# Kernel tuning notes

Hardware: AMD Instinct MI355X
Metric: run time of the kernel (lower is better)

Reference implementation:

```python
import jax, jax.numpy as jnp
import numpy as np

B, S, D, H = 2, 2048, 1024, 16

def setup_inputs() -> dict:
    key = jax.random.key(0)
    ks = jax.random.split(key, 5)
    s = 0.02
    return {
        "x": jax.random.normal(ks[0], (B, S, D), dtype=jnp.float32),
        "Wq": jax.random.normal(ks[1], (D, D), dtype=jnp.float32) * s,
        "bq": jnp.zeros((D,), dtype=jnp.float32),
        "Wk": jax.random.normal(ks[2], (D, D), dtype=jnp.float32) * s,
        "bk": jnp.zeros((D,), dtype=jnp.float32),
        "Wv": jax.random.normal(ks[3], (D, D), dtype=jnp.float32) * s,
        "bv": jnp.zeros((D,), dtype=jnp.float32),
        "Wp": jax.random.normal(ks[4], (D, D), dtype=jnp.float32) * s,
        "bp": jnp.zeros((D,), dtype=jnp.float32),
    }

def reference(x, Wq, bq, Wk, bk, Wv, bv, Wp, bp):
    b, s, d = x.shape
    hd = d // H
    # QKV projections, split into heads: [b, H, s, hd]
    q = (x @ Wq.T + bq).reshape(b, s, H, hd).transpose(0, 2, 1, 3)
    k = (x @ Wk.T + bk).reshape(b, s, H, hd).transpose(0, 2, 1, 3)
    v = (x @ Wv.T + bv).reshape(b, s, H, hd).transpose(0, 2, 1, 3)
    # NOTE: original scales by 1/sqrt(embedding_size), not head_dim
    att = jnp.einsum("bhqd,bhkd->bhqk", q, k) / jnp.sqrt(jnp.float32(d))
    causal = jnp.tril(jnp.ones((s, s), dtype=bool))
    att = jnp.where(causal[None, None], att, -jnp.inf)
    att = jax.nn.softmax(att, axis=-1)
    y = jnp.einsum("bhqk,bhkd->bhqd", att, v)
    y = y.transpose(0, 2, 1, 3).reshape(b, s, d)
    return y @ Wp.T + bp
```

## Files before the change

kernel.cpp:

```cpp
#include <hip/hip_runtime.h>
#include <hip/hip_bf16.h>

#define B_  2
#define S_  2048
#define D_  1024
#define H_  16
#define HD_ 64

typedef float  f32x4 __attribute__((ext_vector_type(4)));
typedef __bf16 bf16x8 __attribute__((ext_vector_type(8)));

__device__ __forceinline__ unsigned short f2bf(float f) {
    __bf16 h = (__bf16)f;
    return __builtin_bit_cast(unsigned short, h);
}
__device__ __forceinline__ float bf2f(unsigned short u) {
    return (float)__builtin_bit_cast(__bf16, u);
}

__device__ __forceinline__ void gload_lds16(const unsigned short* g, unsigned short* l) {
    __builtin_amdgcn_global_load_lds(
        (const __attribute__((address_space(1))) unsigned int*)g,
        (__attribute__((address_space(3))) unsigned int*)l, 16, 0, 0);
}

__global__ __launch_bounds__(256) void cvt5(
    const float* __restrict__ x,  const float* __restrict__ wq,
    const float* __restrict__ wk, const float* __restrict__ wv,
    const float* __restrict__ wp, const float* __restrict__ bq,
    const float* __restrict__ bk, const float* __restrict__ bv,
    unsigned short* __restrict__ xb, unsigned short* __restrict__ wqkv,
    unsigned short* __restrict__ wpb, float* __restrict__ bcat)
{
    const int bid = blockIdx.x;
    if (bid >= 8192) {
        const float* s = (bid == 8192) ? bq : (bid == 8193) ? bk : bv;
        const int i = threadIdx.x * 4;
        *reinterpret_cast<float4*>(bcat + (bid - 8192) * 1024 + i) =
            *reinterpret_cast<const float4*>(s + i);
        return;
    }
    const float* src; unsigned short* dst; int off;
    if (bid < 4096)      { src = x;  dst = xb;              off = bid * 1024; }
    else if (bid < 5120) { src = wq; dst = wqkv;            off = (bid - 4096) * 1024; }
    else if (bid < 6144) { src = wk; dst = wqkv + (1<<20);  off = (bid - 5120) * 1024; }
    else if (bid < 7168) { src = wv; dst = wqkv + (2<<20);  off = (bid - 6144) * 1024; }
    else                 { src = wp; dst = wpb;             off = (bid - 7168) * 1024; }
    const int i = off + threadIdx.x * 4;
    float4 v = *reinterpret_cast<const float4*>(src + i);
    ushort4 o;
    o.x = f2bf(v.x); o.y = f2bf(v.y); o.z = f2bf(v.z); o.w = f2bf(v.w);
    *reinterpret_cast<ushort4*>(dst + i) = o;
}

__global__ __launch_bounds__(256, 3) void gemm128_qkv(
    const unsigned short* __restrict__ A,
    const unsigned short* __restrict__ Bm,
    const float* __restrict__ bias,
    void* __restrict__ C0, void* __restrict__ C1, void* __restrict__ C2,
    int M, int N, int K)
{
    __shared__ unsigned short As[128 * 64];
    __shared__ unsigned short Bs[128 * 64];
    const int tid  = threadIdx.x;
    const int lane = tid & 63;
    const int w    = tid >> 6;
    const int wm   = w >> 1, wn = w & 1;
    const int m0   = blockIdx.x << 7, n0 = blockIdx.y << 7;
    const int l15  = lane & 15, l4 = lane >> 4;
    const int r8   = lane >> 3;
    const int c8   = (lane & 7) << 3;

    f32x4 acc[4][4] = {};

    for (int k0 = 0; k0 < K; k0 += 64) {
        if (k0) __syncthreads();
        #pragma unroll
        for (int i = 0; i < 4; ++i) {
            const int row = i * 32 + w * 8;
            gload_lds16(A  + (size_t)(m0 + row + r8) * K + k0 + c8, As + row * 64);
            gload_lds16(Bm + (size_t)(n0 + row + r8) * K + k0 + c8, Bs + row * 64);
        }
        __syncthreads();
        #pragma unroll
        for (int kk = 0; kk < 2; ++kk) {
            bf16x8 af[4], bf[4];
            #pragma unroll
            for (int mi = 0; mi < 4; ++mi)
                af[mi] = *reinterpret_cast<const bf16x8*>(&As[(wm * 64 + mi * 16 + l15) * 64 + kk * 32 + l4 * 8]);
            #pragma unroll
            for (int ni = 0; ni < 4; ++ni)
                bf[ni] = *reinterpret_cast<const bf16x8*>(&Bs[(wn * 64 + ni * 16 + l15) * 64 + kk * 32 + l4 * 8]);
            #pragma unroll
            for (int mi = 0; mi < 4; ++mi)
                #pragma unroll
                for (int ni = 0; ni < 4; ++ni)
                    acc[mi][ni] = __builtin_amdgcn_mfma_f32_16x16x32_bf16(af[mi], bf[ni], acc[mi][ni], 0, 0, 0);
        }
    }

    const int region = n0 >> 10;
    #pragma unroll
    for (int mi = 0; mi < 4; ++mi) {
        #pragma unroll
        for (int ni = 0; ni < 4; ++ni) {
            const int colg = n0 + wn * 64 + ni * 16 + l15;
            const float bv = bias[colg];
            const int rowb = m0 + wm * 64 + mi * 16 + l4 * 4;
            const int cl = colg & 1023;
            if (region < 2) {
                unsigned short* C = (unsigned short*)(region ? C1 : C0);
                #pragma unroll
                for (int j = 0; j < 4; ++j)
                    C[(size_t)(rowb + j) * 1024 + cl] = f2bf(acc[mi][ni][j] + bv);
            } else {
                ushort4 pk;
                pk.x = f2bf(acc[mi][ni][0] + bv);
                pk.y = f2bf(acc[mi][ni][1] + bv);
                pk.z = f2bf(acc[mi][ni][2] + bv);
                pk.w = f2bf(acc[mi][ni][3] + bv);
                const int bb = rowb >> 11, s = rowb & (S_ - 1);
                unsigned short* vt = (unsigned short*)C2 +
                    ((size_t)(bb * H_ + (cl >> 6)) * HD_ + (cl & 63)) * S_ + s;
                *reinterpret_cast<ushort4*>(vt) = pk;
            }
        }
    }
}

__global__ __launch_bounds__(256, 2) void gemm64_proj(
    const unsigned short* __restrict__ A,
    const unsigned short* __restrict__ Bm,
    const float* __restrict__ bias,
    float* __restrict__ C,
    int M, int N, int K)
{
    __shared__ unsigned short As[64 * 64];
    __shared__ unsigned short Bs[128 * 64];
    const int tid  = threadIdx.x;
    const int lane = tid & 63;
    const int w    = tid >> 6;
    const int m0   = blockIdx.x << 6, n0 = blockIdx.y << 7;
    const int l15  = lane & 15, l4 = lane >> 4;
    const int r8   = lane >> 3;
    const int c8   = (lane & 7) << 3;

    f32x4 acc[4][2] = {};

    for (int k0 = 0; k0 < K; k0 += 64) {
        if (k0) __syncthreads();
        #pragma unroll
        for (int i = 0; i < 6; ++i) {
            const int c = w * 6 + i;
            if (c < 8)
                gload_lds16(A  + (size_t)(m0 + c * 8 + r8) * K + k0 + c8, As + c * 512);
            else
                gload_lds16(Bm + (size_t)(n0 + (c - 8) * 8 + r8) * K + k0 + c8, Bs + (c - 8) * 512);
        }
        __syncthreads();
        #pragma unroll
        for (int kk = 0; kk < 2; ++kk) {
            bf16x8 af[4], bf[2];
            #pragma unroll
            for (int mi = 0; mi < 4; ++mi)
                af[mi] = *reinterpret_cast<const bf16x8*>(&As[(mi * 16 + l15) * 64 + kk * 32 + l4 * 8]);
            #pragma unroll
            for (int ni = 0; ni < 2; ++ni)
                bf[ni] = *reinterpret_cast<const bf16x8*>(&Bs[(w * 32 + ni * 16 + l15) * 64 + kk * 32 + l4 * 8]);
            #pragma unroll
            for (int mi = 0; mi < 4; ++mi)
                #pragma unroll
                for (int ni = 0; ni < 2; ++ni)
                    acc[mi][ni] = __builtin_amdgcn_mfma_f32_16x16x32_bf16(af[mi], bf[ni], acc[mi][ni], 0, 0, 0);
        }
    }

    #pragma unroll
    for (int mi = 0; mi < 4; ++mi) {
        #pragma unroll
        for (int ni = 0; ni < 2; ++ni) {
            const int colg = n0 + w * 32 + ni * 16 + l15;
            const float bv = bias[colg];
            const int rowb = m0 + mi * 16 + l4 * 4;
            #pragma unroll
            for (int j = 0; j < 4; ++j)
                C[(size_t)(rowb + j) * N + colg] = acc[mi][ni][j] + bv;
        }
    }
}

#define SC_ 0.04508422f
__global__ __launch_bounds__(64, 2) void attn8(
    const unsigned short* __restrict__ qb,
    const unsigned short* __restrict__ kb,
    const unsigned short* __restrict__ vt,
    unsigned short* __restrict__ opart,
    float* __restrict__ lpart)
{
    __shared__ unsigned short Plds[32][88];

    const int lane = threadIdx.x;
    const int l15  = lane & 15, l4 = lane >> 4;

    const int bid  = blockIdx.x;
    const int xcd  = bid & 7;
    const int idx  = bid >> 3;
    const int hb   = xcd * 4 + (idx >> 7);
    const int rem  = idx & 127;
    const int sp   = rem >> 6;
    const int j    = rem & 63;
    const int j32  = j & 31;
    const int qi   = ((j >> 5) & 1) ? j32 : 63 - j32;
    const int h    = hb & 15, b = hb >> 4;

    const int q0w  = qi * 32;
    const size_t baseTok = (size_t)b * S_;
    const unsigned short* kgh = kb + baseTok * D_ + h * HD_;
    const unsigned short* vth = vt + (size_t)(b * H_ + h) * HD_ * S_;

    const int nkv  = (q0w + 95) >> 6;
    const int half = (nkv + 1) >> 1;
    const int t0   = sp ? half : 0;
    const int t1   = sp ? nkv  : half;

    bf16x8 qf[2][2];
    #pragma unroll
    for (int m = 0; m < 2; ++m)
        #pragma unroll
        for (int kh = 0; kh < 2; ++kh)
            qf[m][kh] = *reinterpret_cast<const bf16x8*>(
                qb + (baseTok + q0w + m * 16 + l15) * D_ + h * HD_ + kh * 32 + l4 * 8);

    f32x4 o_acc[2][4] = {};
    float l_part[2][4] = {};

    if (t0 < t1) {
        bf16x8 kf[4][2];
        #pragma unroll
        for (int kvb = 0; kvb < 4; ++kvb)
            #pragma unroll
            for (int kh = 0; kh < 2; ++kh)
                kf[kvb][kh] = *reinterpret_cast<const bf16x8*>(
                    kgh + (size_t)(t0 * 64 + kvb * 16 + l15) * D_ + kh * 32 + l4 * 8);

        for (int t = t0; t < t1; ++t) {
            const int kv0 = t << 6;
            const bool last = (t == nkv - 1);

            f32x4 s0[4] = {}, s1[4] = {};
            __builtin_amdgcn_s_setprio(1);
            #pragma unroll
            for (int kvb = 0; kvb < 4; ++kvb)
                #pragma unroll
                for (int kh = 0; kh < 2; ++kh)
                    s0[kvb] = __builtin_amdgcn_mfma_f32_16x16x32_bf16(
                        qf[0][kh], kf[kvb][kh], s0[kvb], 0, 0, 0);
            #pragma unroll
            for (int kvb = 0; kvb < 4; ++kvb)
                #pragma unroll
                for (int kh = 0; kh < 2; ++kh)
                    s1[kvb] = __builtin_amdgcn_mfma_f32_16x16x32_bf16(
                        qf[1][kh], kf[kvb][kh], s1[kvb], 0, 0, 0);
            __builtin_amdgcn_s_setprio(0);

            if (t + 1 < t1) {
                #pragma unroll
                for (int kvb = 0; kvb < 4; ++kvb)
                    #pragma unroll
                    for (int kh = 0; kh < 2; ++kh)
                        kf[kvb][kh] = *reinterpret_cast<const bf16x8*>(
                            kgh + (size_t)(kv0 + 64 + kvb * 16 + l15) * D_ + kh * 32 + l4 * 8);
            }

            bf16x8 vf0[4];
            #pragma unroll
            for (int nb = 0; nb < 4; ++nb)
                vf0[nb] = *reinterpret_cast<const bf16x8*>(
                    vth + (size_t)(nb * 16 + l15) * S_ + kv0 + l4 * 8);

            const int r = l4 * 4;
            if (!last) {
                #pragma unroll
                for (int jj = 0; jj < 4; ++jj) {
                    float p0 = exp2f(s0[0][jj] * SC_), p1 = exp2f(s0[1][jj] * SC_);
                    float p2 = exp2f(s0[2][jj] * SC_), p3 = exp2f(s0[3][jj] * SC_);
                    l_part[0][jj] += (p0 + p1) + (p2 + p3);
                    Plds[r + jj][l15]      = f2bf(p0);
                    Plds[r + jj][16 + l15] = f2bf(p1);
                    Plds[r + jj][32 + l15] = f2bf(p2);
                    Plds[r + jj][48 + l15] = f2bf(p3);
                }
                #pragma unroll
                for (int jj = 0; jj < 4; ++jj) {
                    float p0 = exp2f(s1[0][jj] * SC_), p1 = exp2f(s1[1][jj] * SC_);
                    float p2 = exp2f(s1[2][jj] * SC_), p3 = exp2f(s1[3][jj] * SC_);
                    l_part[1][jj] += (p0 + p1) + (p2 + p3);
                    Plds[16 + r + jj][l15]      = f2bf(p0);
                    Plds[16 + r + jj][16 + l15] = f2bf(p1);
                    Plds[16 + r + jj][32 + l15] = f2bf(p2);
                    Plds[16 + r + jj][48 + l15] = f2bf(p3);
                }
            } else {
                #pragma unroll
                for (int jj = 0; jj < 4; ++jj) {
                    const int rowg = q0w + r + jj;
                    float p[4];
                    #pragma unroll
                    for (int kvb = 0; kvb < 4; ++kvb) {
                        const bool ok = (kv0 + kvb * 16 + l15 <= rowg);
                        p[kvb] = ok ? exp2f(s0[kvb][jj] * SC_) : 0.f;
                        Plds[r + jj][kvb * 16 + l15] = f2bf(p[kvb]);
                    }
                    l_part[0][jj] += (p[0] + p[1]) + (p[2] + p[3]);
                }
                #pragma unroll
                for (int jj = 0; jj < 4; ++jj) {
                    const int rowg = q0w + 16 + r + jj;
                    float p[4];
                    #pragma unroll
                    for (int kvb = 0; kvb < 4; ++kvb) {
                        const bool ok = (kv0 + kvb * 16 + l15 <= rowg);
                        p[kvb] = ok ? exp2f(s1[kvb][jj] * SC_) : 0.f;
                        Plds[16 + r + jj][kvb * 16 + l15] = f2bf(p[kvb]);
                    }
                    l_part[1][jj] += (p[0] + p[1]) + (p[2] + p[3]);
                }
            }

            bf16x8 vf1[4];
            #pragma unroll
            for (int nb = 0; nb < 4; ++nb)
                vf1[nb] = *reinterpret_cast<const bf16x8*>(
                    vth + (size_t)(nb * 16 + l15) * S_ + kv0 + 32 + l4 * 8);

            {
                bf16x8 pf0 = *reinterpret_cast<const bf16x8*>(&Plds[l15][l4 * 8]);
                bf16x8 pf1 = *reinterpret_cast<const bf16x8*>(&Plds[16 + l15][l4 * 8]);
                __builtin_amdgcn_s_setprio(1);
                #pragma unroll
                for (int nb = 0; nb < 4; ++nb) {
                    o_acc[0][nb] = __builtin_amdgcn_mfma_f32_16x16x32_bf16(pf0, vf0[nb], o_acc[0][nb], 0, 0, 0);
                    o_acc[1][nb] = __builtin_amdgcn_mfma_f32_16x16x32_bf16(pf1, vf0[nb], o_acc[1][nb], 0, 0, 0);
                }
                __builtin_amdgcn_s_setprio(0);
            }
            {
                bf16x8 pf0 = *reinterpret_cast<const bf16x8*>(&Plds[l15][32 + l4 * 8]);
                bf16x8 pf1 = *reinterpret_cast<const bf16x8*>(&Plds[16 + l15][32 + l4 * 8]);
                __builtin_amdgcn_s_setprio(1);
                #pragma unroll
                for (int nb = 0; nb < 4; ++nb) {
                    o_acc[0][nb] = __builtin_amdgcn_mfma_f32_16x16x32_bf16(pf0, vf1[nb], o_acc[0][nb], 0, 0, 0);
                    o_acc[1][nb] = __builtin_amdgcn_mfma_f32_16x16x32_bf16(pf1, vf1[nb], o_acc[1][nb], 0, 0, 0);
                }
                __builtin_amdgcn_s_setprio(0);
            }
        }
    }

    const int slot = (hb * 64 + qi) * 2 + sp;
    float l[8];
    #pragma unroll
    for (int m = 0; m < 2; ++m)
        #pragma unroll
        for (int jj = 0; jj < 4; ++jj)
            l[m * 4 + jj] = l_part[m][jj];
    #pragma unroll
    for (int st = 1; st <= 8; st <<= 1) {
        float tv[8];
        #pragma unroll
        for (int i = 0; i < 8; ++i) tv[i] = __shfl_xor(l[i], st);
        #pragma unroll
        for (int i = 0; i < 8; ++i) l[i] += tv[i];
    }
    if (l15 == 0) {
        float* lp = lpart + slot * 32;
        #pragma unroll
        for (int m = 0; m < 2; ++m)
            #pragma unroll
            for (int jj = 0; jj < 4; ++jj)
                lp[m * 16 + l4 * 4 + jj] = l[m * 4 + jj];
    }
    unsigned short* op = opart + (size_t)slot * 2048;
    #pragma unroll
    for (int m = 0; m < 2; ++m)
        #pragma unroll
        for (int nb = 0; nb < 4; ++nb)
            #pragma unroll
            for (int jj = 0; jj < 4; ++jj)
                op[(m * 16 + l4 * 4 + jj) * 64 + nb * 16 + l15] = f2bf(o_acc[m][nb][jj]);
}

__global__ __launch_bounds__(64) void attn_combine(
    const unsigned short* __restrict__ opart,
    const float* __restrict__ lpart,
    unsigned short* __restrict__ yb)
{
    const int g   = blockIdx.x;
    const int hb  = g >> 6, qi = g & 63;
    const int b   = hb >> 4, h = hb & 15;
    const int lane = threadIdx.x;
    const unsigned short* op0 = opart + (size_t)(g * 2) * 2048;
    const unsigned short* op1 = op0 + 2048;
    const float* lp0 = lpart + g * 2 * 32;
    const float* lp1 = lp0 + 32;
    #pragma unroll 4
    for (int row = 0; row < 32; ++row) {
        const float o = bf2f(op0[row * 64 + lane]) + bf2f(op1[row * 64 + lane]);
        const float l = lp0[row] + lp1[row];
        yb[((size_t)(b * S_ + qi * 32 + row)) * D_ + h * HD_ + lane] = f2bf(o / l);
    }
}

extern "C" void kernel_launch(void* const* d_in, const int* in_sizes, int n_in,
                              void* d_out, int out_size, void* d_ws, size_t ws_size,
                              hipStream_t stream)
{
    const float* x  = (const float*)d_in[0];
    const float* Wq = (const float*)d_in[1];
    const float* bq = (const float*)d_in[2];
    const float* Wk = (const float*)d_in[3];
    const float* bk = (const float*)d_in[4];
    const float* Wv = (const float*)d_in[5];
    const float* bv = (const float*)d_in[6];
    const float* Wp = (const float*)d_in[7];
    const float* bp = (const float*)d_in[8];

    char* ws = (char*)d_ws;
    const size_t MB = 1024 * 1024;
    unsigned short* xb    = (unsigned short*)(ws);
    unsigned short* wqkvb = (unsigned short*)(ws + 8 * MB);
    unsigned short* opart = (unsigned short*)(ws);
    unsigned short* qbuf  = (unsigned short*)(ws + 16 * MB);
    unsigned short* kbuf  = (unsigned short*)(ws + 24 * MB);
    unsigned short* vtbf  = (unsigned short*)(ws + 32 * MB);
    unsigned short* ybuf  = (unsigned short*)(ws + 40 * MB);
    unsigned short* wpb   = (unsigned short*)(ws + 48 * MB);
    float*          bcat  = (float*)(ws + 50 * MB);
    float*          lpart = (float*)(ws + 50 * MB + 65536);

    const int M = B_ * S_;

    cvt5<<<8195, 256, 0, stream>>>(x, Wq, Wk, Wv, Wp, bq, bk, bv, xb, wqkvb, wpb, bcat);

    gemm128_qkv<<<dim3(M / 128, 3072 / 128, 1), 256, 0, stream>>>(
        xb, wqkvb, bcat, qbuf, kbuf, vtbf, M, 3072, D_);

    attn8<<<4096, 64, 0, stream>>>(qbuf, kbuf, vtbf, opart, lpart);
    attn_combine<<<2048, 64, 0, stream>>>(opart, lpart, ybuf);

    gemm64_proj<<<dim3(M / 64, D_ / 128, 1), 256, 0, stream>>>(
        ybuf, wpb, bp, (float*)d_out, M, D_, D_);
}
```

Baseline: 235.4 us.

## Balance causal attention work with variable KV splits per query tile

Replaces the fixed two-way KV split per query tile with a variable split: short tiles run unsplit, medium tiles split in two and long tiles in three. Blocks are ordered heaviest-first within each head group. The change also drops the empty split blocks and evens out per-block work to reduce tail imbalance. The combine kernel now sums a variable number of partials, and the V loads for both halves are hoisted together, which raises register pressure.

Result: slower. 252.7 us (+7.3%).

```diff
diff --git a/kernel.cpp b/kernel.cpp
--- a/kernel.cpp
+++ b/kernel.cpp
@@ -190,7 +190,7 @@
 }
 
 #define SC_ 0.04508422f
-__global__ __launch_bounds__(64, 2) void attn8(
+__global__ __launch_bounds__(64, 2) void attn9(
     const unsigned short* __restrict__ qb,
     const unsigned short* __restrict__ kb,
     const unsigned short* __restrict__ vt,
@@ -205,24 +205,25 @@
     const int bid  = blockIdx.x;
     const int xcd  = bid & 7;
     const int idx  = bid >> 3;
-    const int hb   = xcd * 4 + (idx >> 7);
-    const int rem  = idx & 127;
-    const int sp   = rem >> 6;
-    const int j    = rem & 63;
-    const int j32  = j & 31;
-    const int qi   = ((j >> 5) & 1) ? j32 : 63 - j32;
-    const int h    = hb & 15, b = hb >> 4;
+    const int hb   = xcd * 4 + idx / 126;
+    const int srr  = idx % 126;
+    const int slot = 125 - srr;
+    int qi, part, ns;
+    if (slot < 22)      { qi = slot; part = 0; ns = 1; }
+    else if (slot < 66) { const int u = slot - 22; qi = 22 + (u >> 1); part = u & 1; ns = 2; }
+    else                { const int u = slot - 66; const int q3 = u / 3; qi = 44 + q3; part = u - q3 * 3; ns = 3; }
+    const int h = hb & 15, b = hb >> 4;
 
     const int q0w  = qi * 32;
+    const int nkv  = (qi >> 1) + 1;
+    const int len  = nkv / ns, rem = nkv % ns;
+    const int t0   = part * len + (part < rem ? part : rem);
+    const int t1   = t0 + len + (part < rem ? 1 : 0);
+
     const size_t baseTok = (size_t)b * S_;
     const unsigned short* kgh = kb + baseTok * D_ + h * HD_;
     const unsigned short* vth = vt + (size_t)(b * H_ + h) * HD_ * S_;
 
-    const int nkv  = (q0w + 95) >> 6;
-    const int half = (nkv + 1) >> 1;
-    const int t0   = sp ? half : 0;
-    const int t1   = sp ? nkv  : half;
-
     bf16x8 qf[2][2];
     #pragma unroll
     for (int m = 0; m < 2; ++m)
@@ -234,131 +235,127 @@
     f32x4 o_acc[2][4] = {};
     float l_part[2][4] = {};
 
-    if (t0 < t1) {
-        bf16x8 kf[4][2];
+    bf16x8 kf[4][2];
+    #pragma unroll
+    for (int kvb = 0; kvb < 4; ++kvb)
+        #pragma unroll
+        for (int kh = 0; kh < 2; ++kh)
+            kf[kvb][kh] = *reinterpret_cast<const bf16x8*>(
+                kgh + (size_t)(t0 * 64 + kvb * 16 + l15) * D_ + kh * 32 + l4 * 8);
+
+    for (int t = t0; t < t1; ++t) {
+        const int kv0 = t << 6;
+        const bool last = (t == nkv - 1);
+
+        f32x4 s0[4] = {}, s1[4] = {};
+        __builtin_amdgcn_s_setprio(1);
         #pragma unroll
         for (int kvb = 0; kvb < 4; ++kvb)
             #pragma unroll
             for (int kh = 0; kh < 2; ++kh)
-                kf[kvb][kh] = *reinterpret_cast<const bf16x8*>(
-                    kgh + (size_t)(t0 * 64 + kvb * 16 + l15) * D_ + kh * 32 + l4 * 8);
-
-        for (int t = t0; t < t1; ++t) {
-            const int kv0 = t << 6;
-            const bool last = (t == nkv - 1);
-
-            f32x4 s0[4] = {}, s1[4] = {};
+                s0[kvb] = __builtin_amdgcn_mfma_f32_16x16x32_bf16(
+                    qf[0][kh], kf[kvb][kh], s0[kvb], 0, 0, 0);
+        #pragma unroll
+        for (int kvb = 0; kvb < 4; ++kvb)
+            #pragma unroll
+            for (int kh = 0; kh < 2; ++kh)
+                s1[kvb] = __builtin_amdgcn_mfma_f32_16x16x32_bf16(
+                    qf[1][kh], kf[kvb][kh], s1[kvb], 0, 0, 0);
+        __builtin_amdgcn_s_setprio(0);
+
+        if (t + 1 < t1) {
+            #pragma unroll
+            for (int kvb = 0; kvb < 4; ++kvb)
+                #pragma unroll
+                for (int kh = 0; kh < 2; ++kh)
+                    kf[kvb][kh] = *reinterpret_cast<const bf16x8*>(
+                        kgh + (size_t)(kv0 + 64 + kvb * 16 + l15) * D_ + kh * 32 + l4 * 8);
+        }
+
+        bf16x8 vf0[4], vf1[4];
+        #pragma unroll
+        for (int nb = 0; nb < 4; ++nb)
+            vf0[nb] = *reinterpret_cast<const bf16x8*>(
+                vth + (size_t)(nb * 16 + l15) * S_ + kv0 + l4 * 8);
+        #pragma unroll
+        for (int nb = 0; nb < 4; ++nb)
+            vf1[nb] = *reinterpret_cast<const bf16x8*>(
+                vth + (size_t)(nb * 16 + l15) * S_ + kv0 + 32 + l4 * 8);
+
+        const int r = l4 * 4;
+        if (!last) {
+            #pragma unroll
+            for (int jj = 0; jj < 4; ++jj) {
+                float p0 = exp2f(s0[0][jj] * SC_), p1 = exp2f(s0[1][jj] * SC_);
+                float p2 = exp2f(s0[2][jj] * SC_), p3 = exp2f(s0[3][jj] * SC_);
+                l_part[0][jj] += (p0 + p1) + (p2 + p3);
+                Plds[r + jj][l15]      = f2bf(p0);
+                Plds[r + jj][16 + l15] = f2bf(p1);
+                Plds[r + jj][32 + l15] = f2bf(p2);
+                Plds[r + jj][48 + l15] = f2bf(p3);
+            }
+            #pragma unroll
+            for (int jj = 0; jj < 4; ++jj) {
+                float p0 = exp2f(s1[0][jj] * SC_), p1 = exp2f(s1[1][jj] * SC_);
+                float p2 = exp2f(s1[2][jj] * SC_), p3 = exp2f(s1[3][jj] * SC_);
+                l_part[1][jj] += (p0 + p1) + (p2 + p3);
+                Plds[16 + r + jj][l15]      = f2bf(p0);
+                Plds[16 + r + jj][16 + l15] = f2bf(p1);
+                Plds[16 + r + jj][32 + l15] = f2bf(p2);
+                Plds[16 + r + jj][48 + l15] = f2bf(p3);
+            }
+        } else {
+            #pragma unroll
+            for (int jj = 0; jj < 4; ++jj) {
+                const int rowg = q0w + r + jj;
+                float p[4];
+                #pragma unroll
+                for (int kvb = 0; kvb < 4; ++kvb) {
+                    const bool ok = (kv0 + kvb * 16 + l15 <= rowg);
+                    p[kvb] = ok ? exp2f(s0[kvb][jj] * SC_) : 0.f;
+                    Plds[r + jj][kvb * 16 + l15] = f2bf(p[kvb]);
+                }
+                l_part[0][jj] += (p[0] + p[1]) + (p[2] + p[3]);
+            }
+            #pragma unroll
+            for (int jj = 0; jj < 4; ++jj) {
+                const int rowg = q0w + 16 + r + jj;
+                float p[4];
+                #pragma unroll
+                for (int kvb = 0; kvb < 4; ++kvb) {
+                    const bool ok = (kv0 + kvb * 16 + l15 <= rowg);
+                    p[kvb] = ok ? exp2f(s1[kvb][jj] * SC_) : 0.f;
+                    Plds[16 + r + jj][kvb * 16 + l15] = f2bf(p[kvb]);
+                }
+                l_part[1][jj] += (p[0] + p[1]) + (p[2] + p[3]);
+            }
+        }
+
+        {
+            bf16x8 pf0 = *reinterpret_cast<const bf16x8*>(&Plds[l15][l4 * 8]);
+            bf16x8 pf1 = *reinterpret_cast<const bf16x8*>(&Plds[16 + l15][l4 * 8]);
             __builtin_amdgcn_s_setprio(1);
             #pragma unroll
-            for (int kvb = 0; kvb < 4; ++kvb)
-                #pragma unroll
-                for (int kh = 0; kh < 2; ++kh)
-                    s0[kvb] = __builtin_amdgcn_mfma_f32_16x16x32_bf16(
-                        qf[0][kh], kf[kvb][kh], s0[kvb], 0, 0, 0);
-            #pragma unroll
-            for (int kvb = 0; kvb < 4; ++kvb)
-                #pragma unroll
-                for (int kh = 0; kh < 2; ++kh)
-                    s1[kvb] = __builtin_amdgcn_mfma_f32_16x16x32_bf16(
-                        qf[1][kh], kf[kvb][kh], s1[kvb], 0, 0, 0);
+            for (int nb = 0; nb < 4; ++nb) {
+                o_acc[0][nb] = __builtin_amdgcn_mfma_f32_16x16x32_bf16(pf0, vf0[nb], o_acc[0][nb], 0, 0, 0);
+                o_acc[1][nb] = __builtin_amdgcn_mfma_f32_16x16x32_bf16(pf1, vf0[nb], o_acc[1][nb], 0, 0, 0);
+            }
             __builtin_amdgcn_s_setprio(0);
-
-            if (t + 1 < t1) {
-                #pragma unroll
-                for (int kvb = 0; kvb < 4; ++kvb)
-                    #pragma unroll
-                    for (int kh = 0; kh < 2; ++kh)
-                        kf[kvb][kh] = *reinterpret_cast<const bf16x8*>(
-                            kgh + (size_t)(kv0 + 64 + kvb * 16 + l15) * D_ + kh * 32 + l4 * 8);
-            }
-
-            bf16x8 vf0[4];
-            #pragma unroll
-            for (int nb = 0; nb < 4; ++nb)
-                vf0[nb] = *reinterpret_cast<const bf16x8*>(
-                    vth + (size_t)(nb * 16 + l15) * S_ + kv0 + l4 * 8);
-
-            const int r = l4 * 4;
-            if (!last) {
-                #pragma unroll
-                for (int jj = 0; jj < 4; ++jj) {
-                    float p0 = exp2f(s0[0][jj] * SC_), p1 = exp2f(s0[1][jj] * SC_);
-                    float p2 = exp2f(s0[2][jj] * SC_), p3 = exp2f(s0[3][jj] * SC_);
-                    l_part[0][jj] += (p0 + p1) + (p2 + p3);
-                    Plds[r + jj][l15]      = f2bf(p0);
-                    Plds[r + jj][16 + l15] = f2bf(p1);
-                    Plds[r + jj][32 + l15] = f2bf(p2);
-                    Plds[r + jj][48 + l15] = f2bf(p3);
-                }
-                #pragma unroll
-                for (int jj = 0; jj < 4; ++jj) {
-                    float p0 = exp2f(s1[0][jj] * SC_), p1 = exp2f(s1[1][jj] * SC_);
-                    float p2 = exp2f(s1[2][jj] * SC_), p3 = exp2f(s1[3][jj] * SC_);
-                    l_part[1][jj] += (p0 + p1) + (p2 + p3);
-                    Plds[16 + r + jj][l15]      = f2bf(p0);
-                    Plds[16 + r + jj][16 + l15] = f2bf(p1);
-                    Plds[16 + r + jj][32 + l15] = f2bf(p2);
-                    Plds[16 + r + jj][48 + l15] = f2bf(p3);
-                }
-            } else {
-                #pragma unroll
-                for (int jj = 0; jj < 4; ++jj) {
-                    const int rowg = q0w + r + jj;
-                    float p[4];
-                    #pragma unroll
-                    for (int kvb = 0; kvb < 4; ++kvb) {
-                        const bool ok = (kv0 + kvb * 16 + l15 <= rowg);
-                        p[kvb] = ok ? exp2f(s0[kvb][jj] * SC_) : 0.f;
-                        Plds[r + jj][kvb * 16 + l15] = f2bf(p[kvb]);
-                    }
-                    l_part[0][jj] += (p[0] + p[1]) + (p[2] + p[3]);
-                }
-                #pragma unroll
-                for (int jj = 0; jj < 4; ++jj) {
-                    const int rowg = q0w + 16 + r + jj;
-                    float p[4];
-                    #pragma unroll
-                    for (int kvb = 0; kvb < 4; ++kvb) {
-                        const bool ok = (kv0 + kvb * 16 + l15 <= rowg);
-                        p[kvb] = ok ? exp2f(s1[kvb][jj] * SC_) : 0.f;
-                        Plds[16 + r + jj][kvb * 16 + l15] = f2bf(p[kvb]);
-                    }
-                    l_part[1][jj] += (p[0] + p[1]) + (p[2] + p[3]);
-                }
-            }
-
-            bf16x8 vf1[4];
-            #pragma unroll
-            for (int nb = 0; nb < 4; ++nb)
-                vf1[nb] = *reinterpret_cast<const bf16x8*>(
-                    vth + (size_t)(nb * 16 + l15) * S_ + kv0 + 32 + l4 * 8);
-
-            {
-                bf16x8 pf0 = *reinterpret_cast<const bf16x8*>(&Plds[l15][l4 * 8]);
-                bf16x8 pf1 = *reinterpret_cast<const bf16x8*>(&Plds[16 + l15][l4 * 8]);
-                __builtin_amdgcn_s_setprio(1);
-                #pragma unroll
-                for (int nb = 0; nb < 4; ++nb) {
-                    o_acc[0][nb] = __builtin_amdgcn_mfma_f32_16x16x32_bf16(pf0, vf0[nb], o_acc[0][nb], 0, 0, 0);
-                    o_acc[1][nb] = __builtin_amdgcn_mfma_f32_16x16x32_bf16(pf1, vf0[nb], o_acc[1][nb], 0, 0, 0);
-                }
-                __builtin_amdgcn_s_setprio(0);
-            }
-            {
-                bf16x8 pf0 = *reinterpret_cast<const bf16x8*>(&Plds[l15][32 + l4 * 8]);
-                bf16x8 pf1 = *reinterpret_cast<const bf16x8*>(&Plds[16 + l15][32 + l4 * 8]);
-                __builtin_amdgcn_s_setprio(1);
-                #pragma unroll
-                for (int nb = 0; nb < 4; ++nb) {
-                    o_acc[0][nb] = __builtin_amdgcn_mfma_f32_16x16x32_bf16(pf0, vf1[nb], o_acc[0][nb], 0, 0, 0);
-                    o_acc[1][nb] = __builtin_amdgcn_mfma_f32_16x16x32_bf16(pf1, vf1[nb], o_acc[1][nb], 0, 0, 0);
-                }
-                __builtin_amdgcn_s_setprio(0);
-            }
-        }
-    }
-
-    const int slot = (hb * 64 + qi) * 2 + sp;
+        }
+        {
+            bf16x8 pf0 = *reinterpret_cast<const bf16x8*>(&Plds[l15][32 + l4 * 8]);
+            bf16x8 pf1 = *reinterpret_cast<const bf16x8*>(&Plds[16 + l15][32 + l4 * 8]);
+            __builtin_amdgcn_s_setprio(1);
+            #pragma unroll
+            for (int nb = 0; nb < 4; ++nb) {
+                o_acc[0][nb] = __builtin_amdgcn_mfma_f32_16x16x32_bf16(pf0, vf1[nb], o_acc[0][nb], 0, 0, 0);
+                o_acc[1][nb] = __builtin_amdgcn_mfma_f32_16x16x32_bf16(pf1, vf1[nb], o_acc[1][nb], 0, 0, 0);
+            }
+            __builtin_amdgcn_s_setprio(0);
+        }
+    }
+
+    const int gslot = hb * 126 + slot;
     float l[8];
     #pragma unroll
     for (int m = 0; m < 2; ++m)
@@ -374,14 +371,14 @@
         for (int i = 0; i < 8; ++i) l[i] += tv[i];
     }
     if (l15 == 0) {
-        float* lp = lpart + slot * 32;
+        float* lp = lpart + gslot * 32;
         #pragma unroll
         for (int m = 0; m < 2; ++m)
             #pragma unroll
             for (int jj = 0; jj < 4; ++jj)
                 lp[m * 16 + l4 * 4 + jj] = l[m * 4 + jj];
     }
-    unsigned short* op = opart + (size_t)slot * 2048;
+    unsigned short* op = opart + (size_t)gslot * 2048;
     #pragma unroll
     for (int m = 0; m < 2; ++m)
         #pragma unroll
@@ -400,14 +397,18 @@
     const int hb  = g >> 6, qi = g & 63;
     const int b   = hb >> 4, h = hb & 15;
     const int lane = threadIdx.x;
-    const unsigned short* op0 = opart + (size_t)(g * 2) * 2048;
-    const unsigned short* op1 = op0 + 2048;
-    const float* lp0 = lpart + g * 2 * 32;
-    const float* lp1 = lp0 + 32;
+    int base, ns;
+    if (qi < 22)      { base = qi;                      ns = 1; }
+    else if (qi < 44) { base = 22 + ((qi - 22) << 1);   ns = 2; }
+    else              { base = 66 + (qi - 44) * 3;      ns = 3; }
+    const int gb = hb * 126 + base;
     #pragma unroll 4
     for (int row = 0; row < 32; ++row) {
-        const float o = bf2f(op0[row * 64 + lane]) + bf2f(op1[row * 64 + lane]);
-        const float l = lp0[row] + lp1[row];
+        float o = 0.f, l = 0.f;
+        for (int s = 0; s < ns; ++s) {
+            o += bf2f(opart[(size_t)(gb + s) * 2048 + row * 64 + lane]);
+            l += lpart[(gb + s) * 32 + row];
+        }
         yb[((size_t)(b * S_ + qi * 32 + row)) * D_ + h * HD_ + lane] = f2bf(o / l);
     }
 }
@@ -446,7 +447,7 @@
     gemm128_qkv<<<dim3(M / 128, 3072 / 128, 1), 256, 0, stream>>>(
         xb, wqkvb, bcat, qbuf, kbuf, vtbf, M, 3072, D_);
 
-    attn8<<<4096, 64, 0, stream>>>(qbuf, kbuf, vtbf, opart, lpart);
+    attn9<<<4032, 64, 0, stream>>>(qbuf, kbuf, vtbf, opart, lpart);
     attn_combine<<<2048, 64, 0, stream>>>(opart, lpart, ybuf);
 
     gemm64_proj<<<dim3(M / 64, D_ / 128, 1), 256, 0, stream>>>(
```

## Drop split-KV attention and combine kernel, normalize in-kernel; remap GEMM block order

Applied to the files above, without the earlier changes.

Attention no longer splits each query tile's KV range across two blocks. Each block now processes the full causal range and writes the normalized bf16 output directly, which removes the partial-output and sum buffers and the separate combine kernel. V fragments are prefetched one tile ahead, like K. Both GEMMs switch to a 1D grid with an XCD-aware or column-interleaved block index mapping meant to improve L2 reuse. The cost is half as many attention blocks, each doing longer and more uneven work, which may hurt load balance and latency hiding.

After: 217.4 us. 7.7% less time.

```diff
diff --git a/kernel.cpp b/kernel.cpp
--- a/kernel.cpp
+++ b/kernel.cpp
@@ -13,9 +13,6 @@
 __device__ __forceinline__ unsigned short f2bf(float f) {
     __bf16 h = (__bf16)f;
     return __builtin_bit_cast(unsigned short, h);
-}
-__device__ __forceinline__ float bf2f(unsigned short u) {
-    return (float)__builtin_bit_cast(__bf16, u);
 }
 
 __device__ __forceinline__ void gload_lds16(const unsigned short* g, unsigned short* l) {
@@ -66,7 +63,8 @@
     const int lane = tid & 63;
     const int w    = tid >> 6;
     const int wm   = w >> 1, wn = w & 1;
-    const int m0   = blockIdx.x << 7, n0 = blockIdx.y << 7;
+    const int g    = (blockIdx.x & 7) * 96 + (blockIdx.x >> 3);
+    const int m0   = (g & 31) << 7, n0 = (g >> 5) << 7;
     const int l15  = lane & 15, l4 = lane >> 4;
     const int r8   = lane >> 3;
     const int c8   = (lane & 7) << 3;
@@ -140,7 +138,8 @@
     const int tid  = threadIdx.x;
     const int lane = tid & 63;
     const int w    = tid >> 6;
-    const int m0   = blockIdx.x << 6, n0 = blockIdx.y << 7;
+    const int m0   = (blockIdx.x >> 3) << 6;
+    const int n0   = (blockIdx.x & 7) << 7;
     const int l15  = lane & 15, l4 = lane >> 4;
     const int r8   = lane >> 3;
     const int c8   = (lane & 7) << 3;
@@ -190,12 +189,11 @@
 }
 
 #define SC_ 0.04508422f
-__global__ __launch_bounds__(64, 2) void attn8(
+__global__ __launch_bounds__(64, 2) void attn10(
     const unsigned short* __restrict__ qb,
     const unsigned short* __restrict__ kb,
     const unsigned short* __restrict__ vt,
-    unsigned short* __restrict__ opart,
-    float* __restrict__ lpart)
+    unsigned short* __restrict__ yb)
 {
     __shared__ unsigned short Plds[32][88];
 
@@ -205,12 +203,9 @@
     const int bid  = blockIdx.x;
     const int xcd  = bid & 7;
     const int idx  = bid >> 3;
-    const int hb   = xcd * 4 + (idx >> 7);
-    const int rem  = idx & 127;
-    const int sp   = rem >> 6;
-    const int j    = rem & 63;
-    const int j32  = j & 31;
-    const int qi   = ((j >> 5) & 1) ? j32 : 63 - j32;
+    const int hb   = xcd * 4 + (idx >> 6);
+    const int j32  = idx & 31;
+    const int qi   = ((idx >> 5) & 1) ? j32 : 63 - j32;
     const int h    = hb & 15, b = hb >> 4;
 
     const int q0w  = qi * 32;
@@ -218,11 +213,6 @@
     const unsigned short* kgh = kb + baseTok * D_ + h * HD_;
     const unsigned short* vth = vt + (size_t)(b * H_ + h) * HD_ * S_;
 
-    const int nkv  = (q0w + 95) >> 6;
-    const int half = (nkv + 1) >> 1;
-    const int t0   = sp ? half : 0;
-    const int t1   = sp ? nkv  : half;
-
     bf16x8 qf[2][2];
     #pragma unroll
     for (int m = 0; m < 2; ++m)
@@ -234,131 +224,133 @@
     f32x4 o_acc[2][4] = {};
     float l_part[2][4] = {};
 
-    if (t0 < t1) {
-        bf16x8 kf[4][2];
+    const int nkv = (q0w + 95) >> 6;
+
+    bf16x8 kf[4][2], vf[2][4];
+    #pragma unroll
+    for (int kvb = 0; kvb < 4; ++kvb)
+        #pragma unroll
+        for (int kh = 0; kh < 2; ++kh)
+            kf[kvb][kh] = *reinterpret_cast<const bf16x8*>(
+                kgh + (size_t)(kvb * 16 + l15) * D_ + kh * 32 + l4 * 8);
+    #pragma unroll
+    for (int kvh = 0; kvh < 2; ++kvh)
+        #pragma unroll
+        for (int nb = 0; nb < 4; ++nb)
+            vf[kvh][nb] = *reinterpret_cast<const bf16x8*>(
+                vth + (size_t)(nb * 16 + l15) * S_ + kvh * 32 + l4 * 8);
+
+    for (int t = 0; t < nkv; ++t) {
+        const int kv0 = t << 6;
+        const bool last = (t == nkv - 1);
+
+        f32x4 s0[4] = {}, s1[4] = {};
+        __builtin_amdgcn_s_setprio(1);
         #pragma unroll
         for (int kvb = 0; kvb < 4; ++kvb)
             #pragma unroll
             for (int kh = 0; kh < 2; ++kh)
-                kf[kvb][kh] = *reinterpret_cast<const bf16x8*>(
-                    kgh + (size_t)(t0 * 64 + kvb * 16 + l15) * D_ + kh * 32 + l4 * 8);
-
-        for (int t = t0; t < t1; ++t) {
-            const int kv0 = t << 6;
-            const bool last = (t == nkv - 1);
-
-            f32x4 s0[4] = {}, s1[4] = {};
+                s0[kvb] = __builtin_amdgcn_mfma_f32_16x16x32_bf16(
+                    qf[0][kh], kf[kvb][kh], s0[kvb], 0, 0, 0);
+        #pragma unroll
+        for (int kvb = 0; kvb < 4; ++kvb)
+            #pragma unroll
+            for (int kh = 0; kh < 2; ++kh)
+                s1[kvb] = __builtin_amdgcn_mfma_f32_16x16x32_bf16(
+                    qf[1][kh], kf[kvb][kh], s1[kvb], 0, 0, 0);
+        __builtin_amdgcn_s_setprio(0);
+
+        if (t + 1 < nkv) {
+            #pragma unroll
+            for (int kvb = 0; kvb < 4; ++kvb)
+                #pragma unroll
+                for (int kh = 0; kh < 2; ++kh)
+                    kf[kvb][kh] = *reinterpret_cast<const bf16x8*>(
+                        kgh + (size_t)(kv0 + 64 + kvb * 16 + l15) * D_ + kh * 32 + l4 * 8);
+        }
+
+        const int r = l4 * 4;
+        if (!last) {
+            #pragma unroll
+            for (int jj = 0; jj < 4; ++jj) {
+                float p0 = exp2f(s0[0][jj] * SC_), p1 = exp2f(s0[1][jj] * SC_);
+                float p2 = exp2f(s0[2][jj] * SC_), p3 = exp2f(s0[3][jj] * SC_);
+                l_part[0][jj] += (p0 + p1) + (p2 + p3);
+                Plds[r + jj][l15]      = f2bf(p0);
+                Plds[r + jj][16 + l15] = f2bf(p1);
+                Plds[r + jj][32 + l15] = f2bf(p2);
+                Plds[r + jj][48 + l15] = f2bf(p3);
+            }
+            #pragma unroll
+            for (int jj = 0; jj < 4; ++jj) {
+                float p0 = exp2f(s1[0][jj] * SC_), p1 = exp2f(s1[1][jj] * SC_);
+                float p2 = exp2f(s1[2][jj] * SC_), p3 = exp2f(s1[3][jj] * SC_);
+                l_part[1][jj] += (p0 + p1) + (p2 + p3);
+                Plds[16 + r + jj][l15]      = f2bf(p0);
+                Plds[16 + r + jj][16 + l15] = f2bf(p1);
+                Plds[16 + r + jj][32 + l15] = f2bf(p2);
+                Plds[16 + r + jj][48 + l15] = f2bf(p3);
+            }
+        } else {
+            #pragma unroll
+            for (int jj = 0; jj < 4; ++jj) {
+                const int rowg = q0w + r + jj;
+                float p[4];
+                #pragma unroll
+                for (int kvb = 0; kvb < 4; ++kvb) {
+                    const bool ok = (kv0 + kvb * 16 + l15 <= rowg);
+                    p[kvb] = ok ? exp2f(s0[kvb][jj] * SC_) : 0.f;
+                    Plds[r + jj][kvb * 16 + l15] = f2bf(p[kvb]);
+                }
+                l_part[0][jj] += (p[0] + p[1]) + (p[2] + p[3]);
+            }
+            #pragma unroll
+            for (int jj = 0; jj < 4; ++jj) {
+                const int rowg = q0w + 16 + r + jj;
+                float p[4];
+                #pragma unroll
+                for (int kvb = 0; kvb < 4; ++kvb) {
+                    const bool ok = (kv0 + kvb * 16 + l15 <= rowg);
+                    p[kvb] = ok ? exp2f(s1[kvb][jj] * SC_) : 0.f;
+                    Plds[16 + r + jj][kvb * 16 + l15] = f2bf(p[kvb]);
+                }
+                l_part[1][jj] += (p[0] + p[1]) + (p[2] + p[3]);
+            }
+        }
+
+        {
+            bf16x8 pf0 = *reinterpret_cast<const bf16x8*>(&Plds[l15][l4 * 8]);
+            bf16x8 pf1 = *reinterpret_cast<const bf16x8*>(&Plds[16 + l15][l4 * 8]);
             __builtin_amdgcn_s_setprio(1);
             #pragma unroll
-            for (int kvb = 0; kvb < 4; ++kvb)
-                #pragma unroll
-                for (int kh = 0; kh < 2; ++kh)
-                    s0[kvb] = __builtin_amdgcn_mfma_f32_16x16x32_bf16(
-                        qf[0][kh], kf[kvb][kh], s0[kvb], 0, 0, 0);
-            #pragma unroll
-            for (int kvb = 0; kvb < 4; ++kvb)
-                #pragma unroll
-                for (int kh = 0; kh < 2; ++kh)
-                    s1[kvb] = __builtin_amdgcn_mfma_f32_16x16x32_bf16(
-                        qf[1][kh], kf[kvb][kh], s1[kvb], 0, 0, 0);
+            for (int nb = 0; nb < 4; ++nb) {
+                o_acc[0][nb] = __builtin_amdgcn_mfma_f32_16x16x32_bf16(pf0, vf[0][nb], o_acc[0][nb], 0, 0, 0);
+                o_acc[1][nb] = __builtin_amdgcn_mfma_f32_16x16x32_bf16(pf1, vf[0][nb], o_acc[1][nb], 0, 0, 0);
+            }
             __builtin_amdgcn_s_setprio(0);
-
-            if (t + 1 < t1) {
-                #pragma unroll
-                for (int kvb = 0; kvb < 4; ++kvb)
-                    #pragma unroll
-                    for (int kh = 0; kh < 2; ++kh)
-                        kf[kvb][kh] = *reinterpret_cast<const bf16x8*>(
-                            kgh + (size_t)(kv0 + 64 + kvb * 16 + l15) * D_ + kh * 32 + l4 * 8);
-            }
-
-            bf16x8 vf0[4];
-            #pragma unroll
-            for (int nb = 0; nb < 4; ++nb)
-                vf0[nb] = *reinterpret_cast<const bf16x8*>(
-                    vth + (size_t)(nb * 16 + l15) * S_ + kv0 + l4 * 8);
-
-            const int r = l4 * 4;
-            if (!last) {
-                #pragma unroll
-                for (int jj = 0; jj < 4; ++jj) {
-                    float p0 = exp2f(s0[0][jj] * SC_), p1 = exp2f(s0[1][jj] * SC_);
-                    float p2 = exp2f(s0[2][jj] * SC_), p3 = exp2f(s0[3][jj] * SC_);
-                    l_part[0][jj] += (p0 + p1) + (p2 + p3);
-                    Plds[r + jj][l15]      = f2bf(p0);
-                    Plds[r + jj][16 + l15] = f2bf(p1);
-                    Plds[r + jj][32 + l15] = f2bf(p2);
-                    Plds[r + jj][48 + l15] = f2bf(p3);
-                }
-                #pragma unroll
-                for (int jj = 0; jj < 4; ++jj) {
-                    float p0 = exp2f(s1[0][jj] * SC_), p1 = exp2f(s1[1][jj] * SC_);
-                    float p2 = exp2f(s1[2][jj] * SC_), p3 = exp2f(s1[3][jj] * SC_);
-                    l_part[1][jj] += (p0 + p1) + (p2 + p3);
-                    Plds[16 + r + jj][l15]      = f2bf(p0);
-                    Plds[16 + r + jj][16 + l15] = f2bf(p1);
-                    Plds[16 + r + jj][32 + l15] = f2bf(p2);
-                    Plds[16 + r + jj][48 + l15] = f2bf(p3);
-                }
-            } else {
-                #pragma unroll
-                for (int jj = 0; jj < 4; ++jj) {
-                    const int rowg = q0w + r + jj;
-                    float p[4];
-                    #pragma unroll
-                    for (int kvb = 0; kvb < 4; ++kvb) {
-                        const bool ok = (kv0 + kvb * 16 + l15 <= rowg);
-                        p[kvb] = ok ? exp2f(s0[kvb][jj] * SC_) : 0.f;
-                        Plds[r + jj][kvb * 16 + l15] = f2bf(p[kvb]);
-                    }
-                    l_part[0][jj] += (p[0] + p[1]) + (p[2] + p[3]);
-                }
-                #pragma unroll
-                for (int jj = 0; jj < 4; ++jj) {
-                    const int rowg = q0w + 16 + r + jj;
-                    float p[4];
-                    #pragma unroll
-                    for (int kvb = 0; kvb < 4; ++kvb) {
-                        const bool ok = (kv0 + kvb * 16 + l15 <= rowg);
-                        p[kvb] = ok ? exp2f(s1[kvb][jj] * SC_) : 0.f;
-                        Plds[16 + r + jj][kvb * 16 + l15] = f2bf(p[kvb]);
-                    }
-                    l_part[1][jj] += (p[0] + p[1]) + (p[2] + p[3]);
-                }
-            }
-
-            bf16x8 vf1[4];
-            #pragma unroll
-            for (int nb = 0; nb < 4; ++nb)
-                vf1[nb] = *reinterpret_cast<const bf16x8*>(
-                    vth + (size_t)(nb * 16 + l15) * S_ + kv0 + 32 + l4 * 8);
-
-            {
-                bf16x8 pf0 = *reinterpret_cast<const bf16x8*>(&Plds[l15][l4 * 8]);
-                bf16x8 pf1 = *reinterpret_cast<const bf16x8*>(&Plds[16 + l15][l4 * 8]);
-                __builtin_amdgcn_s_setprio(1);
-                #pragma unroll
-                for (int nb = 0; nb < 4; ++nb) {
-                    o_acc[0][nb] = __builtin_amdgcn_mfma_f32_16x16x32_bf16(pf0, vf0[nb], o_acc[0][nb], 0, 0, 0);
-                    o_acc[1][nb] = __builtin_amdgcn_mfma_f32_16x16x32_bf16(pf1, vf0[nb], o_acc[1][nb], 0, 0, 0);
-                }
-                __builtin_amdgcn_s_setprio(0);
-            }
-            {
-                bf16x8 pf0 = *reinterpret_cast<const bf16x8*>(&Plds[l15][32 + l4 * 8]);
-                bf16x8 pf1 = *reinterpret_cast<const bf16x8*>(&Plds[16 + l15][32 + l4 * 8]);
-                __builtin_amdgcn_s_setprio(1);
-                #pragma unroll
-                for (int nb = 0; nb < 4; ++nb) {
-                    o_acc[0][nb] = __builtin_amdgcn_mfma_f32_16x16x32_bf16(pf0, vf1[nb], o_acc[0][nb], 0, 0, 0);
-                    o_acc[1][nb] = __builtin_amdgcn_mfma_f32_16x16x32_bf16(pf1, vf1[nb], o_acc[1][nb], 0, 0, 0);
-                }
-                __builtin_amdgcn_s_setprio(0);
-            }
-        }
-    }
-
-    const int slot = (hb * 64 + qi) * 2 + sp;
+        }
+        {
+            bf16x8 pf0 = *reinterpret_cast<const bf16x8*>(&Plds[l15][32 + l4 * 8]);
+            bf16x8 pf1 = *reinterpret_cast<const bf16x8*>(&Plds[16 + l15][32 + l4 * 8]);
+            __builtin_amdgcn_s_setprio(1);
+            #pragma unroll
+            for (int nb = 0; nb < 4; ++nb) {
+                o_acc[0][nb] = __builtin_amdgcn_mfma_f32_16x16x32_bf16(pf0, vf[1][nb], o_acc[0][nb], 0, 0, 0);
+                o_acc[1][nb] = __builtin_amdgcn_mfma_f32_16x16x32_bf16(pf1, vf[1][nb], o_acc[1][nb], 0, 0, 0);
+            }
+            __builtin_amdgcn_s_setprio(0);
+        }
+
+        if (t + 1 < nkv) {
+            #pragma unroll
+            for (int kvh = 0; kvh < 2; ++kvh)
+                #pragma unroll
+                for (int nb = 0; nb < 4; ++nb)
+                    vf[kvh][nb] = *reinterpret_cast<const bf16x8*>(
+                        vth + (size_t)(nb * 16 + l15) * S_ + kv0 + 64 + kvh * 32 + l4 * 8);
+        }
+    }
+
     float l[8];
     #pragma unroll
     for (int m = 0; m < 2; ++m)
@@ -373,42 +365,17 @@
         #pragma unroll
         for (int i = 0; i < 8; ++i) l[i] += tv[i];
     }
-    if (l15 == 0) {
-        float* lp = lpart + slot * 32;
-        #pragma unroll
-        for (int m = 0; m < 2; ++m)
-            #pragma unroll
-            for (int jj = 0; jj < 4; ++jj)
-                lp[m * 16 + l4 * 4 + jj] = l[m * 4 + jj];
-    }
-    unsigned short* op = opart + (size_t)slot * 2048;
-    #pragma unroll
-    for (int m = 0; m < 2; ++m)
-        #pragma unroll
-        for (int nb = 0; nb < 4; ++nb)
-            #pragma unroll
-            for (int jj = 0; jj < 4; ++jj)
-                op[(m * 16 + l4 * 4 + jj) * 64 + nb * 16 + l15] = f2bf(o_acc[m][nb][jj]);
-}
-
-__global__ __launch_bounds__(64) void attn_combine(
-    const unsigned short* __restrict__ opart,
-    const float* __restrict__ lpart,
-    unsigned short* __restrict__ yb)
-{
-    const int g   = blockIdx.x;
-    const int hb  = g >> 6, qi = g & 63;
-    const int b   = hb >> 4, h = hb & 15;
-    const int lane = threadIdx.x;
-    const unsigned short* op0 = opart + (size_t)(g * 2) * 2048;
-    const unsigned short* op1 = op0 + 2048;
-    const float* lp0 = lpart + g * 2 * 32;
-    const float* lp1 = lp0 + 32;
-    #pragma unroll 4
-    for (int row = 0; row < 32; ++row) {
-        const float o = bf2f(op0[row * 64 + lane]) + bf2f(op1[row * 64 + lane]);
-        const float l = lp0[row] + lp1[row];
-        yb[((size_t)(b * S_ + qi * 32 + row)) * D_ + h * HD_ + lane] = f2bf(o / l);
+    #pragma unroll
+    for (int m = 0; m < 2; ++m) {
+        #pragma unroll
+        for (int jj = 0; jj < 4; ++jj) {
+            const float inv = 1.0f / l[m * 4 + jj];
+            const int rowg = q0w + m * 16 + l4 * 4 + jj;
+            unsigned short* yp = yb + (baseTok + rowg) * D_ + h * HD_ + l15;
+            #pragma unroll
+            for (int nb = 0; nb < 4; ++nb)
+                yp[nb * 16] = f2bf(o_acc[m][nb][jj] * inv);
+        }
     }
 }
 
@@ -430,25 +397,22 @@
     const size_t MB = 1024 * 1024;
     unsigned short* xb    = (unsigned short*)(ws);
     unsigned short* wqkvb = (unsigned short*)(ws + 8 * MB);
-    unsigned short* opart = (unsigned short*)(ws);
     unsigned short* qbuf  = (unsigned short*)(ws + 16 * MB);
     unsigned short* kbuf  = (unsigned short*)(ws + 24 * MB);
     unsigned short* vtbf  = (unsigned short*)(ws + 32 * MB);
     unsigned short* ybuf  = (unsigned short*)(ws + 40 * MB);
     unsigned short* wpb   = (unsigned short*)(ws + 48 * MB);
     float*          bcat  = (float*)(ws + 50 * MB);
-    float*          lpart = (float*)(ws + 50 * MB + 65536);
 
     const int M = B_ * S_;
 
     cvt5<<<8195, 256, 0, stream>>>(x, Wq, Wk, Wv, Wp, bq, bk, bv, xb, wqkvb, wpb, bcat);
 
-    gemm128_qkv<<<dim3(M / 128, 3072 / 128, 1), 256, 0, stream>>>(
+    gemm128_qkv<<<768, 256, 0, stream>>>(
         xb, wqkvb, bcat, qbuf, kbuf, vtbf, M, 3072, D_);
 
-    attn8<<<4096, 64, 0, stream>>>(qbuf, kbuf, vtbf, opart, lpart);
-    attn_combine<<<2048, 64, 0, stream>>>(opart, lpart, ybuf);
-
-    gemm64_proj<<<dim3(M / 64, D_ / 128, 1), 256, 0, stream>>>(
+    attn10<<<2048, 64, 0, stream>>>(qbuf, kbuf, vtbf, ybuf);
+
+    gemm64_proj<<<512, 256, 0, stream>>>(
         ybuf, wpb, bp, (float*)d_out, M, D_, D_);
 }
```
